# Performance work log

Hardware: AMD Instinct MI355X
Metric: run time of the kernel (lower is better)

Reference implementation:

```python
import jax, jax.numpy as jnp
import numpy as np

N = 4096
HID = 256
H = 4
D = HID // H  # 64
EDGE_DIM = 16
DEG = 32
E = N * DEG
EPS = 1e-5


def _layer_norm(x, g, b):
    m = jnp.mean(x, axis=-1, keepdims=True)
    v = jnp.mean((x - m) ** 2, axis=-1, keepdims=True)
    return (x - m) * jax.lax.rsqrt(v + EPS) * g + b


def setup_inputs() -> dict:
    key = jax.random.key(0)
    ks = jax.random.split(key, 16)
    s = 1.0 / np.sqrt(HID)
    x = jax.random.normal(ks[0], (N, HID), dtype=jnp.float32)
    # ring graph: every node is a src with DEG distinct neighbors -> no empty
    # softmax rows, no duplicate (src, dst) pairs
    src = jnp.repeat(jnp.arange(N, dtype=jnp.int64), DEG)
    dst = (src + jnp.tile(jnp.arange(1, DEG + 1, dtype=jnp.int64), N)) % N
    edge_index = jnp.stack([src, dst], axis=0)
    edge_attr = jax.random.normal(ks[1], (E, EDGE_DIM), dtype=jnp.float32)
    inp = {
        "x": x,
        "edge_index": edge_index,
        "edge_attr": edge_attr,
        "Wq": jax.random.uniform(ks[2], (HID, HID), jnp.float32, -s, s),
        "bq": jnp.zeros((HID,), jnp.float32),
        "Wk": jax.random.uniform(ks[3], (HID, HID), jnp.float32, -s, s),
        "bk": jnp.zeros((HID,), jnp.float32),
        "Wv": jax.random.uniform(ks[4], (HID, HID), jnp.float32, -s, s),
        "bv": jnp.zeros((HID,), jnp.float32),
        "Wo": jax.random.uniform(ks[5], (HID, HID), jnp.float32, -s, s),
        "bo": jnp.zeros((HID,), jnp.float32),
        "We": jax.random.uniform(ks[6], (EDGE_DIM, H), jnp.float32, -1.0 / np.sqrt(EDGE_DIM), 1.0 / np.sqrt(EDGE_DIM)),
        "be": jnp.zeros((H,), jnp.float32),
        "g1": jnp.ones((HID,), jnp.float32),
        "b1": jnp.zeros((HID,), jnp.float32),
        "g2": jnp.ones((HID,), jnp.float32),
        "b2": jnp.zeros((HID,), jnp.float32),
        "Wf1": jax.random.uniform(ks[7], (HID, 4 * HID), jnp.float32, -s, s),
        "bf1": jnp.zeros((4 * HID,), jnp.float32),
        "Wf2": jax.random.uniform(ks[8], (4 * HID, HID), jnp.float32, -1.0 / np.sqrt(4 * HID), 1.0 / np.sqrt(4 * HID)),
        "bf2": jnp.zeros((HID,), jnp.float32),
    }
    return inp


def reference(x, edge_index, edge_attr, Wq, bq, Wk, bk, Wv, bv, Wo, bo,
              We, be, g1, b1, g2, b2, Wf1, bf1, Wf2, bf2):
    src, dst = edge_index[0], edge_index[1]
    q = (x @ Wq + bq).reshape(N, H, D)
    k = (x @ Wk + bk).reshape(N, H, D)
    v = (x @ Wv + bv).reshape(N, H, D)
    edge_bias = edge_attr @ We + be                       # [E, H]
    dot = jnp.sum(q[src] * k[dst], axis=-1) / np.sqrt(D)  # [E, H]
    total_bias = dot + edge_bias                          # [E, H]
    # dense (H, N, N) logits, -inf everywhere except the E edges (as in the
    # original module)
    logits = jnp.full((H, N, N), -jnp.inf, dtype=x.dtype)
    logits = logits.at[:, src, dst].set(total_bias.T)
    attn = jax.nn.softmax(logits, axis=-1)                # [H, N, N]
    out = jnp.einsum('hnm,mhd->nhd', attn, v).reshape(N, HID)
    out = out @ Wo + bo
    x = _layer_norm(x + out, g1, b1)
    ffn = jax.nn.relu(x @ Wf1 + bf1) @ Wf2 + bf2
    x = _layer_norm(x + ffn, g2, b2)
    return x
```

## Files before the change

kernel.cpp:

```cpp
#include <hip/hip_runtime.h>
#include <cstddef>

#define N_NODES 4096
#define HIDDEN  256
#define NHEAD   4
#define DHEAD   64
#define EDGE_DIM 16
#define DEG     32
#define NEDGE   (N_NODES * DEG)
#define LN_EPS  1e-5f
#define QKV_STRIDE 768
#define KV_WIN  47

typedef short  s16x8 __attribute__((ext_vector_type(8)));
typedef float  f32x4 __attribute__((ext_vector_type(4)));
typedef unsigned short u16x8 __attribute__((ext_vector_type(8)));
typedef unsigned short u16x4 __attribute__((ext_vector_type(4)));

__device__ __forceinline__ unsigned short f2b(float f) {
    union { float f; unsigned u; } c{f};
    unsigned u = c.u;
    return (unsigned short)((u + 0x7fffu + ((u >> 16) & 1u)) >> 16);
}
__device__ __forceinline__ float b2f(unsigned short s) {
    union { unsigned u; float f; } c;
    c.u = ((unsigned)s) << 16;
    return c.f;
}
__device__ __forceinline__ int xcd_swz(int bid, int total) {
    const int q = total >> 3;
    return (bid & 7) * q + (bid >> 3);
}

__device__ __forceinline__ void pack_tile(const float* __restrict__ src,
                                          unsigned short* __restrict__ dst,
                                          int K, int Nn, int tt, int rowoff,
                                          float (*tile)[65], int tid) {
    const int tk = K / 64;
    const int k0 = (tt % tk) * 64, n0 = (tt / tk) * 64;

    const int kk = tid >> 2, nq = (tid & 3) * 16;
#pragma unroll
    for (int i = 0; i < 16; i += 4) {
        float4 vv = *(const float4*)&src[(size_t)(k0 + kk) * Nn + n0 + nq + i];
        tile[kk][nq + i + 0] = vv.x;
        tile[kk][nq + i + 1] = vv.y;
        tile[kk][nq + i + 2] = vv.z;
        tile[kk][nq + i + 3] = vv.w;
    }
    __syncthreads();
    const int nn = tid >> 2, kq = (tid & 3) * 16;
    unsigned short tmp[16];
#pragma unroll
    for (int i = 0; i < 16; ++i) tmp[i] = f2b(tile[kq + i][nn]);
    unsigned short* drow = dst + (size_t)(rowoff + n0 + nn) * K + k0 + kq;
    *(u16x8*)(drow + 0) = *(u16x8*)&tmp[0];
    *(u16x8*)(drow + 8) = *(u16x8*)&tmp[8];
}

__global__ __launch_bounds__(256) void pack_kernel(
    const float* __restrict__ Wq, const float* __restrict__ Wk,
    const float* __restrict__ Wv,
    const float* __restrict__ bq, const float* __restrict__ bk,
    const float* __restrict__ bv,
    unsigned short* __restrict__ Wqkv_t, float* __restrict__ bias768) {
    const int b = blockIdx.x;
    const int tid = threadIdx.x;
    __shared__ float tile[64][65];

    if (b < 48) {
        int m = b / 16, tt = b % 16;
        const float* src = (m == 0) ? Wq : ((m == 1) ? Wk : Wv);
        pack_tile(src, Wqkv_t, 256, 256, tt, m * 256, tile, tid);
    } else {
        bias768[tid]       = bq[tid];
        bias768[256 + tid] = bk[tid];
        bias768[512 + tid] = bv[tid];
    }
}

__global__ __launch_bounds__(256) void gemm_qkv(const float* __restrict__ X,
                                                const unsigned short* __restrict__ Bt,
                                                const float* __restrict__ bias,
                                                unsigned short* __restrict__ Cout,
                                                const float* __restrict__ Wo,
                                                const float* __restrict__ Wf1,
                                                const float* __restrict__ Wf2,
                                                unsigned short* __restrict__ Wo_t,
                                                unsigned short* __restrict__ Wf1_t,
                                                unsigned short* __restrict__ Wf2_t) {
    __shared__ __align__(16) char smem[64 * 65 * 4];
    const int bid = blockIdx.x;
    const int tid = threadIdx.x;

    if (bid >= 768) {
        float (*tile)[65] = (float(*)[65])smem;
        const int b2 = bid - 768;
        if (b2 < 16)       pack_tile(Wo,  Wo_t,  256,  256,  b2,      0, tile, tid);
        else if (b2 < 80)  pack_tile(Wf1, Wf1_t, 256,  1024, b2 - 16, 0, tile, tid);
        else               pack_tile(Wf2, Wf2_t, 1024, 256,  b2 - 80, 0, tile, tid);
        return;
    }

    unsigned short* sA = (unsigned short*)smem;
    unsigned short* sB = sA + 64 * 64;
    const int wave = tid >> 6, lane = tid & 63;
    const int b2 = xcd_swz(bid, 768);
    const int row0 = (b2 / 12) * 64, col0 = (b2 % 12) * 64;
    const int wr = wave >> 1, wc = wave & 1;

    f32x4 acc[2][2] = {};

    const int lo0 = tid * 16, lo1 = lo0 + 4096;
    const int r0 = lo0 >> 7, c0 = lo0 & 127;
    const int r1 = lo1 >> 7, c1 = lo1 & 127;
    const int so0 = (lo0 & ~127) | (c0 ^ ((r0 & 7) << 4));
    const int so1 = (lo1 & ~127) | (c1 ^ ((r1 & 7) << 4));

    const int ar  = tid >> 2;
    const int akb = (tid & 3) * 16;
    const int acb = akb * 2;
    const int axr = (ar & 7) << 4;
    const int aso0 = (ar * 128) | ((acb +  0) ^ axr);
    const int aso1 = (ar * 128) | ((acb + 16) ^ axr);

    float4 f0, f1, f2v, f3;
    s16x8 b0r, b1r;

#define QKV_LOAD(KT)                                                          \
    {                                                                         \
        const float* Ap = X + (size_t)(row0 + ar) * 256 + (KT) * 64 + akb;    \
        f0  = *(const float4*)(Ap + 0);                                       \
        f1  = *(const float4*)(Ap + 4);                                       \
        f2v = *(const float4*)(Ap + 8);                                       \
        f3  = *(const float4*)(Ap + 12);                                      \
        const char* Bb = (const char*)Bt + ((size_t)col0 * 256 + (KT) * 64) * 2; \
        b0r = *(const s16x8*)(Bb + (size_t)r0 * 512 + c0);                    \
        b1r = *(const s16x8*)(Bb + (size_t)r1 * 512 + c1);                    \
    }

    QKV_LOAD(0);
#pragma unroll
    for (int kt = 0; kt < 4; ++kt) {
        if (kt) __syncthreads();
        u16x8 pa0 = {f2b(f0.x), f2b(f0.y), f2b(f0.z), f2b(f0.w),
                     f2b(f1.x), f2b(f1.y), f2b(f1.z), f2b(f1.w)};
        u16x8 pa1 = {f2b(f2v.x), f2b(f2v.y), f2b(f2v.z), f2b(f2v.w),
                     f2b(f3.x), f2b(f3.y), f2b(f3.z), f2b(f3.w)};
        *(u16x8*)((char*)sA + aso0) = pa0;
        *(u16x8*)((char*)sA + aso1) = pa1;
        *(s16x8*)((char*)sB + so0) = b0r;
        *(s16x8*)((char*)sB + so1) = b1r;
        __syncthreads();
        if (kt < 3) QKV_LOAD(kt + 1);

        const char* sAc = (const char*)sA;
        const char* sBc = (const char*)sB;
#pragma unroll
        for (int kk = 0; kk < 64; kk += 32) {
            const int koffb = (kk + ((lane >> 4) << 3)) * 2;
            s16x8 a[2], bfr[2];
#pragma unroll
            for (int m = 0; m < 2; ++m) {
                const int r = wr * 32 + m * 16 + (lane & 15);
                int off = r * 128 + koffb;
                off ^= (r & 7) << 4;
                a[m] = *(const s16x8*)(sAc + off);
            }
#pragma unroll
            for (int n = 0; n < 2; ++n) {
                const int c = wc * 32 + n * 16 + (lane & 15);
                int off = c * 128 + koffb;
                off ^= (c & 7) << 4;
                bfr[n] = *(const s16x8*)(sBc + off);
            }
#pragma unroll
            for (int m = 0; m < 2; ++m)
#pragma unroll
                for (int n = 0; n < 2; ++n)
                    acc[m][n] = __builtin_amdgcn_mfma_f32_16x16x32_bf16(
                        a[m], bfr[n], acc[m][n], 0, 0, 0);
        }
    }
#undef QKV_LOAD

    const int crow = row0 + wr * 32 + ((lane >> 4) << 2);
    const int ccol = col0 + wc * 32 + (lane & 15);
#pragma unroll
    for (int n = 0; n < 2; ++n) {
        const int c = ccol + n * 16;
        const float bv = bias[c];
#pragma unroll
        for (int m = 0; m < 2; ++m)
#pragma unroll
            for (int j = 0; j < 4; ++j)
                Cout[(size_t)(crow + m * 16 + j) * QKV_STRIDE + c] =
                    f2b(acc[m][n][j] + bv);
    }
}

template <int K, bool RELU, bool OUTB>
__global__ __launch_bounds__(256) void gemm_mfma(const unsigned short* __restrict__ A,
                                                 const unsigned short* __restrict__ Bt,
                                                 const float* __restrict__ bias,
                                                 void* __restrict__ Cout,
                                                 int Nn, int nct, int total) {
    constexpr int NT = K / 64;
    __shared__ unsigned short sA[64 * 64];
    __shared__ unsigned short sB[64 * 64];
    const int tid = threadIdx.x;
    const int wave = tid >> 6, lane = tid & 63;
    const int b2 = xcd_swz(blockIdx.x, total);
    const int row0 = (b2 / nct) * 64, col0 = (b2 % nct) * 64;
    const int wr = wave >> 1, wc = wave & 1;

    f32x4 acc[2][2] = {};

    const int lo0 = tid * 16;
    const int lo1 = lo0 + 4096;
    const int r0 = lo0 >> 7, c0 = lo0 & 127;
    const int r1 = lo1 >> 7, c1 = lo1 & 127;
    const int so0 = (lo0 & ~127) | (c0 ^ ((r0 & 7) << 4));
    const int so1 = (lo1 & ~127) | (c1 ^ ((r1 & 7) << 4));

    s16x8 a0r, a1r, b0r, b1r;

#define GM_LOAD(KT)                                                           \
    {                                                                         \
        const char* Ab = (const char*)A + ((size_t)row0 * K + (KT) * 64) * 2; \
        const char* Bb = (const char*)Bt + ((size_t)col0 * K + (KT) * 64) * 2;\
        a0r = *(const s16x8*)(Ab + (size_t)r0 * (K * 2) + c0);                \
        a1r = *(const s16x8*)(Ab + (size_t)r1 * (K * 2) + c1);                \
        b0r = *(const s16x8*)(Bb + (size_t)r0 * (K * 2) + c0);                \
        b1r = *(const s16x8*)(Bb + (size_t)r1 * (K * 2) + c1);                \
    }

    GM_LOAD(0);
#pragma unroll
    for (int kt = 0; kt < NT; ++kt) {
        if (kt) __syncthreads();
        *(s16x8*)((char*)sA + so0) = a0r;
        *(s16x8*)((char*)sA + so1) = a1r;
        *(s16x8*)((char*)sB + so0) = b0r;
        *(s16x8*)((char*)sB + so1) = b1r;
        __syncthreads();
        if (kt + 1 < NT) GM_LOAD(kt + 1);

        const char* sAc = (const char*)sA;
        const char* sBc = (const char*)sB;
#pragma unroll
        for (int kk = 0; kk < 64; kk += 32) {
            const int koffb = (kk + ((lane >> 4) << 3)) * 2;
            s16x8 a[2], bfr[2];
#pragma unroll
            for (int m = 0; m < 2; ++m) {
                const int r = wr * 32 + m * 16 + (lane & 15);
                int off = r * 128 + koffb;
                off ^= (r & 7) << 4;
                a[m] = *(const s16x8*)(sAc + off);
            }
#pragma unroll
            for (int n = 0; n < 2; ++n) {
                const int c = wc * 32 + n * 16 + (lane & 15);
                int off = c * 128 + koffb;
                off ^= (c & 7) << 4;
                bfr[n] = *(const s16x8*)(sBc + off);
            }
#pragma unroll
            for (int m = 0; m < 2; ++m)
#pragma unroll
                for (int n = 0; n < 2; ++n)
                    acc[m][n] = __builtin_amdgcn_mfma_f32_16x16x32_bf16(
                        a[m], bfr[n], acc[m][n], 0, 0, 0);
        }
    }
#undef GM_LOAD

    const int crow = row0 + wr * 32 + ((lane >> 4) << 2);
    const int ccol = col0 + wc * 32 + (lane & 15);
#pragma unroll
    for (int n = 0; n < 2; ++n) {
        const int c = ccol + n * 16;
        const float bv = bias[c];
#pragma unroll
        for (int m = 0; m < 2; ++m) {
#pragma unroll
            for (int j = 0; j < 4; ++j) {
                const int r = crow + m * 16 + j;
                float v = acc[m][n][j] + bv;
                if (RELU) v = fmaxf(v, 0.f);
                if (OUTB)
                    ((unsigned short*)Cout)[(size_t)r * Nn + c] = f2b(v);
                else
                    ((float*)Cout)[(size_t)r * Nn + c] = v;
            }
        }
    }
}

__global__ __launch_bounds__(256) void gemm_partial(const unsigned short* __restrict__ A,
                                                    const unsigned short* __restrict__ Bt,
                                                    float* __restrict__ part) {
    constexpr int KF = 1024;
    __shared__ unsigned short sA[64 * 64];
    __shared__ unsigned short sB[64 * 64];
    const int tid = threadIdx.x;
    const int wave = tid >> 6, lane = tid & 63;
    const int b2 = xcd_swz(blockIdx.x, 512);
    const int z = b2 >> 8;
    const int rem = b2 & 255;
    const int row0 = (rem >> 2) * 64, col0 = (rem & 3) * 64;
    const int wr = wave >> 1, wc = wave & 1;

    f32x4 acc[2][2] = {};

    const int lo0 = tid * 16;
    const int lo1 = lo0 + 4096;
    const int r0 = lo0 >> 7, c0 = lo0 & 127;
    const int r1 = lo1 >> 7, c1 = lo1 & 127;
    const int so0 = (lo0 & ~127) | (c0 ^ ((r0 & 7) << 4));
    const int so1 = (lo1 & ~127) | (c1 ^ ((r1 & 7) << 4));

    const char* Abase = (const char*)A + ((size_t)row0 * KF + z * 512) * 2;
    const char* Bbase = (const char*)Bt + ((size_t)col0 * KF + z * 512) * 2;

    s16x8 a0r, a1r, b0r, b1r;

#define GP_LOAD(KT)                                                           \
    {                                                                         \
        a0r = *(const s16x8*)(Abase + (KT) * 128 + (size_t)r0 * (KF * 2) + c0); \
        a1r = *(const s16x8*)(Abase + (KT) * 128 + (size_t)r1 * (KF * 2) + c1); \
        b0r = *(const s16x8*)(Bbase + (KT) * 128 + (size_t)r0 * (KF * 2) + c0); \
        b1r = *(const s16x8*)(Bbase + (KT) * 128 + (size_t)r1 * (KF * 2) + c1); \
    }

    GP_LOAD(0);
#pragma unroll
    for (int kt = 0; kt < 8; ++kt) {
        if (kt) __syncthreads();
        *(s16x8*)((char*)sA + so0) = a0r;
        *(s16x8*)((char*)sA + so1) = a1r;
        *(s16x8*)((char*)sB + so0) = b0r;
        *(s16x8*)((char*)sB + so1) = b1r;
        __syncthreads();
        if (kt + 1 < 8) GP_LOAD(kt + 1);

        const char* sAc = (const char*)sA;
        const char* sBc = (const char*)sB;
#pragma unroll
        for (int kk = 0; kk < 64; kk += 32) {
            const int koffb = (kk + ((lane >> 4) << 3)) * 2;
            s16x8 a[2], bfr[2];
#pragma unroll
            for (int m = 0; m < 2; ++m) {
                const int r = wr * 32 + m * 16 + (lane & 15);
                int off = r * 128 + koffb;
                off ^= (r & 7) << 4;
                a[m] = *(const s16x8*)(sAc + off);
            }
#pragma unroll
            for (int n = 0; n < 2; ++n) {
                const int c = wc * 32 + n * 16 + (lane & 15);
                int off = c * 128 + koffb;
                off ^= (c & 7) << 4;
                bfr[n] = *(const s16x8*)(sBc + off);
            }
#pragma unroll
            for (int m = 0; m < 2; ++m)
#pragma unroll
                for (int n = 0; n < 2; ++n)
                    acc[m][n] = __builtin_amdgcn_mfma_f32_16x16x32_bf16(
                        a[m], bfr[n], acc[m][n], 0, 0, 0);
        }
    }
#undef GP_LOAD

    const int crow = row0 + wr * 32 + ((lane >> 4) << 2);
    const int ccol = col0 + wc * 32 + (lane & 15);
    float* pz = part + (size_t)z * N_NODES * HIDDEN;
#pragma unroll
    for (int n = 0; n < 2; ++n) {
        const int c = ccol + n * 16;
#pragma unroll
        for (int m = 0; m < 2; ++m)
#pragma unroll
            for (int j = 0; j < 4; ++j)
                pz[(size_t)(crow + m * 16 + j) * HIDDEN + c] = acc[m][n][j];
    }
}

__global__ __launch_bounds__(256) void ln2_reduce(const float* __restrict__ part,
                                                  const float* __restrict__ y,
                                                  const float* __restrict__ bf2,
                                                  const float* __restrict__ g2,
                                                  const float* __restrict__ b2,
                                                  float* __restrict__ out) {
    const int tid = threadIdx.x;
    const int row = blockIdx.x * 16 + (tid >> 4);
    const int cb = (tid & 15) * 16;
    const size_t rb = (size_t)row * HIDDEN;
    constexpr size_t ZS = (size_t)N_NODES * HIDDEN;

    float vals[16];
#pragma unroll
    for (int q = 0; q < 4; ++q) {
        const int c = cb + q * 4;
        float4 vy = *(const float4*)&y[rb + c];
        float4 vb = *(const float4*)&bf2[c];
        float4 s0 = *(const float4*)&part[0 * ZS + rb + c];
        float4 s1 = *(const float4*)&part[1 * ZS + rb + c];
        vals[q * 4 + 0] = vy.x + vb.x + s0.x + s1.x;
        vals[q * 4 + 1] = vy.y + vb.y + s0.y + s1.y;
        vals[q * 4 + 2] = vy.z + vb.z + s0.z + s1.z;
        vals[q * 4 + 3] = vy.w + vb.w + s0.w + s1.w;
    }
    float sm = 0.f, sq = 0.f;
#pragma unroll
    for (int i = 0; i < 16; ++i) { sm += vals[i]; sq = fmaf(vals[i], vals[i], sq); }
#pragma unroll
    for (int off = 8; off >= 1; off >>= 1) {
        sm += __shfl_xor(sm, off);
        sq += __shfl_xor(sq, off);
    }
    const float mean = sm * (1.f / HIDDEN);
    const float var  = sq * (1.f / HIDDEN) - mean * mean;
    const float inv  = rsqrtf(var + LN_EPS);
#pragma unroll
    for (int q = 0; q < 4; ++q) {
        const int c = cb + q * 4;
        float4 vg = *(const float4*)&g2[c];
        float4 vbb = *(const float4*)&b2[c];
        float4 o;
        o.x = (vals[q * 4 + 0] - mean) * inv * vg.x + vbb.x;
        o.y = (vals[q * 4 + 1] - mean) * inv * vg.y + vbb.y;
        o.z = (vals[q * 4 + 2] - mean) * inv * vg.z + vbb.z;
        o.w = (vals[q * 4 + 3] - mean) * inv * vg.w + vbb.w;
        *(float4*)&out[rb + c] = o;
    }
}

__global__ __launch_bounds__(512) void attn_oproj_ln(
    const unsigned short* __restrict__ qkv,
    const int* __restrict__ edge_dst,
    const float* __restrict__ edge_attr,
    const float* __restrict__ We, const float* __restrict__ be,
    const unsigned short* __restrict__ Wo_t,
    const float* __restrict__ bo,
    const float* __restrict__ x,
    const float* __restrict__ g, const float* __restrict__ b,
    float* __restrict__ y, unsigned short* __restrict__ yb) {
    __shared__ float sQ[16][260];
    __shared__ float sP[16][NHEAD][DEG];
    __shared__ int   sDst[16][DEG];
    __shared__ float sWe[EDGE_DIM * NHEAD];
    __shared__ unsigned short sKV[2][KV_WIN * 256];
    __shared__ unsigned short sA[16 * 256];
    __shared__ unsigned short sB[2][256 * 64];
    __shared__ float rs[16][8], rq[16][8];

    const int tid = threadIdx.x;
    const int wave = tid >> 6, lane = tid & 63;
    const int n0 = blockIdx.x * 16;

    {
        const int r = tid >> 5, e = (tid & 31) * 8;
        u16x8 v = *(const u16x8*)(qkv + (size_t)(n0 + r) * QKV_STRIDE + e);
#pragma unroll
        for (int i = 0; i < 8; ++i) sQ[r][e + i] = b2f(v[i]);
    }
    for (int t = tid; t < 2 * KV_WIN * 32; t += 512) {
        const int half = (t >= KV_WIN * 32) ? 1 : 0;
        const int tt = t - half * (KV_WIN * 32);
        const int rr = tt >> 5, c16 = tt & 31;
        const int gsrc = (n0 + 1 + rr) & (N_NODES - 1);
        u16x8 v = *(const u16x8*)(qkv + (size_t)gsrc * QKV_STRIDE +
                                  (half ? 512 : 256) + c16 * 8);
        const int so = rr * 512 + ((c16 ^ (rr & 7)) * 16);
        *(u16x8*)((char*)sKV[half] + so) = v;
    }
    if (tid < EDGE_DIM * NHEAD) sWe[tid] = We[tid];
    __syncthreads();

    {
        const int node = tid >> 5, j = tid & 31;
        const int dstj = edge_dst[(n0 + node) * DEG + j];
        sDst[node][j] = dstj;
        const int idx = (dstj - n0 - 1) & (N_NODES - 1);
        const char* krow = (const char*)sKV[0] + idx * 512;
        const int swz = (idx & 7);
        float lg[4];
#pragma unroll
        for (int h = 0; h < 4; ++h) {
            float dot = 0.f;
            const float* qh = &sQ[node][h * 64];
#pragma unroll
            for (int q8 = 0; q8 < 8; ++q8) {
                const int c16 = h * 8 + q8;
                u16x8 kv = *(const u16x8*)(krow + ((c16 ^ swz) * 16));
#pragma unroll
                for (int d = 0; d < 8; ++d)
                    dot = fmaf(qh[q8 * 8 + d], b2f(kv[d]), dot);
            }
            lg[h] = dot * 0.125f + be[h];
        }
        const float* ea_ = edge_attr + (size_t)((n0 + node) * DEG + j) * EDGE_DIM;
#pragma unroll
        for (int c = 0; c < EDGE_DIM; ++c) {
            const float eav = ea_[c];
#pragma unroll
            for (int h = 0; h < 4; ++h)
                lg[h] = fmaf(eav, sWe[c * NHEAD + h], lg[h]);
        }
#pragma unroll
        for (int h = 0; h < 4; ++h) {
            float mx = lg[h];
#pragma unroll
            for (int off = 16; off >= 1; off >>= 1)
                mx = fmaxf(mx, __shfl_xor(mx, off));
            float p = __expf(lg[h] - mx);
            float sum = p;
#pragma unroll
            for (int off = 16; off >= 1; off >>= 1)
                sum += __shfl_xor(sum, off);
            sP[node][h][j] = p / sum;
        }
    }
    __syncthreads();

    {
        const int node = tid >> 5, oct = tid & 31;
        const int h = oct >> 3;
        const int chunk = oct;
        float acc8[8] = {};
#pragma unroll 8
        for (int j = 0; j < DEG; ++j) {
            const float p = sP[node][h][j];
            const int idx = (sDst[node][j] - n0 - 1) & (N_NODES - 1);
            u16x8 vv = *(const u16x8*)((const char*)sKV[1] + idx * 512 +
                                       ((chunk ^ (idx & 7)) * 16));
#pragma unroll
            for (int i = 0; i < 8; ++i) acc8[i] = fmaf(p, b2f(vv[i]), acc8[i]);
        }
        u16x8 pk;
#pragma unroll
        for (int i = 0; i < 8; ++i) pk[i] = f2b(acc8[i]);
        const int so = node * 512 + ((oct * 16) ^ ((node & 7) << 4));
        *(u16x8*)((char*)sA + so) = pk;
    }

    s16x8 breg[4];
#define WO_LOAD(KT)                                                           \
    {                                                                         \
        _Pragma("unroll")                                                     \
        for (int p = 0; p < 4; ++p) {                                         \
            const int lo = tid * 16 + p * 8192;                               \
            const int r = lo >> 7, c = lo & 127;                              \
            breg[p] = *(const s16x8*)((const char*)Wo_t + (size_t)r * 512 +   \
                                      (KT) * 128 + c);                        \
        }                                                                     \
    }
#define WO_STORE(BUF)                                                         \
    {                                                                         \
        _Pragma("unroll")                                                     \
        for (int p = 0; p < 4; ++p) {                                         \
            const int lo = tid * 16 + p * 8192;                               \
            const int r = lo >> 7, c = lo & 127;                              \
            const int so = (lo & ~127) | (c ^ ((r & 7) << 4));                \
            *(s16x8*)((char*)sB[BUF] + so) = breg[p];                         \
        }                                                                     \
    }

    WO_LOAD(0);
    WO_STORE(0);
    __syncthreads();

    f32x4 acc[2] = {};
#pragma unroll
    for (int kt = 0; kt < 4; ++kt) {
        if (kt + 1 < 4) WO_LOAD(kt + 1);

        const char* sBc = (const char*)sB[kt & 1];
#pragma unroll
        for (int kk = 0; kk < 64; kk += 32) {
            const int lk = ((lane >> 4) << 3);
            s16x8 a;
            {
                const int r = lane & 15;
                const int koffb = (kt * 64 + kk + lk) * 2;
                a = *(const s16x8*)((const char*)sA + r * 512 +
                                    (koffb ^ ((r & 7) << 4)));
            }
            s16x8 bfr[2];
            const int boffb = (kk + lk) * 2;
#pragma unroll
            for (int n = 0; n < 2; ++n) {
                const int c = wave * 32 + n * 16 + (lane & 15);
                bfr[n] = *(const s16x8*)(sBc + c * 128 + (boffb ^ ((c & 7) << 4)));
            }
#pragma unroll
            for (int n = 0; n < 2; ++n)
                acc[n] = __builtin_amdgcn_mfma_f32_16x16x32_bf16(a, bfr[n], acc[n], 0, 0, 0);
        }

        if (kt + 1 < 4) {
            WO_STORE((kt + 1) & 1);
            __syncthreads();
        }
    }
#undef WO_LOAD
#undef WO_STORE

    const int rbase = ((lane >> 4) << 2);
    const int cbase = wave * 32 + (lane & 15);

    float sm[4] = {}, sq_[4] = {};
#pragma unroll
    for (int n = 0; n < 2; ++n) {
        const int c = cbase + n * 16;
        const float bv = bo[c];
#pragma unroll
        for (int j = 0; j < 4; ++j) {
            const int r = rbase + j;
            float v = acc[n][j] + bv + x[(size_t)(n0 + r) * HIDDEN + c];
            acc[n][j] = v;
            sm[j] += v;
            sq_[j] = fmaf(v, v, sq_[j]);
        }
    }
#pragma unroll
    for (int off = 8; off >= 1; off >>= 1) {
#pragma unroll
        for (int j = 0; j < 4; ++j) {
            sm[j] += __shfl_xor(sm[j], off);
            sq_[j] += __shfl_xor(sq_[j], off);
        }
    }
    if ((lane & 15) == 0) {
#pragma unroll
        for (int j = 0; j < 4; ++j) {
            rs[rbase + j][wave] = sm[j];
            rq[rbase + j][wave] = sq_[j];
        }
    }
    __syncthreads();

#pragma unroll
    for (int j = 0; j < 4; ++j) {
        const int r = rbase + j;
        float tot = 0.f, totq = 0.f;
#pragma unroll
        for (int w = 0; w < 8; ++w) { tot += rs[r][w]; totq += rq[r][w]; }
        const float mean = tot * (1.f / HIDDEN);
        const float var  = totq * (1.f / HIDDEN) - mean * mean;
        const float inv  = rsqrtf(var + LN_EPS);
#pragma unroll
        for (int n = 0; n < 2; ++n) {
            const int c = cbase + n * 16;
            const float res = (acc[n][j] - mean) * inv * g[c] + b[c];
            y[(size_t)(n0 + r) * HIDDEN + c] = res;
            yb[(size_t)(n0 + r) * HIDDEN + c] = f2b(res);
        }
    }
}

extern "C" void kernel_launch(void* const* d_in, const int* in_sizes, int n_in,
                              void* d_out, int out_size, void* d_ws, size_t ws_size,
                              hipStream_t stream) {
    const float* x   = (const float*)d_in[0];
    const int*   ei  = (const int*)d_in[1];
    const float* ea  = (const float*)d_in[2];
    const float* Wq  = (const float*)d_in[3];
    const float* bq  = (const float*)d_in[4];
    const float* Wk  = (const float*)d_in[5];
    const float* bk  = (const float*)d_in[6];
    const float* Wv  = (const float*)d_in[7];
    const float* bv  = (const float*)d_in[8];
    const float* Wo  = (const float*)d_in[9];
    const float* bo  = (const float*)d_in[10];
    const float* We  = (const float*)d_in[11];
    const float* be  = (const float*)d_in[12];
    const float* g1  = (const float*)d_in[13];
    const float* b1  = (const float*)d_in[14];
    const float* g2  = (const float*)d_in[15];
    const float* b2  = (const float*)d_in[16];
    const float* Wf1 = (const float*)d_in[17];
    const float* bf1 = (const float*)d_in[18];
    const float* Wf2 = (const float*)d_in[19];
    const float* bf2 = (const float*)d_in[20];

    char* W = (char*)d_ws;
    unsigned short* Wqkv_t  = (unsigned short*)(W + (2u << 20));
    unsigned short* Wo_t    = (unsigned short*)(W + (2u << 20) + 384 * 1024);
    unsigned short* Wf1_t   = (unsigned short*)(W + (2u << 20) + 512 * 1024);
    unsigned short* Wf2_t   = (unsigned short*)(W + (2u << 20) + 1024 * 1024);
    float*          bias768 = (float*)(W + (2u << 20) + 1536 * 1024);
    unsigned short* qkvb    = (unsigned short*)(W + (4u << 20));
    unsigned short* h1b     = (unsigned short*)(W + (4u << 20));
    float*          y       = (float*)(W + (12u << 20));
    unsigned short* yb      = (unsigned short*)(W + (16u << 20));
    float*          part    = (float*)(W + (20u << 20));

    const dim3 blk(256);

    pack_kernel<<<49, blk, 0, stream>>>(Wq, Wk, Wv, bq, bk, bv, Wqkv_t, bias768);

    gemm_qkv<<<912, blk, 0, stream>>>(x, Wqkv_t, bias768, qkvb,
                                      Wo, Wf1, Wf2, Wo_t, Wf1_t, Wf2_t);

    attn_oproj_ln<<<N_NODES / 16, dim3(512), 0, stream>>>(
        qkvb, ei + NEDGE, ea, We, be, Wo_t, bo, x, g1, b1, y, yb);

    gemm_mfma<256, true, true><<<1024, blk, 0, stream>>>(
        yb, Wf1_t, bf1, h1b, 4 * HIDDEN, 16, 1024);

    gemm_partial<<<512, blk, 0, stream>>>(h1b, Wf2_t, part);

    ln2_reduce<<<N_NODES / 16, blk, 0, stream>>>(part, y, bf2, g2, b2, (float*)d_out);
}
```

Baseline: 55.54 us.

## Move weight packing to pack kernel, widen FFN1 tiles, finer LN2 rows

All weight transposes (Wo, Wf1, Wf2) now happen in the pack kernel instead of extra blocks inside the QKV GEMM, so the QKV GEMM gets a smaller LDS footprint and only launches GEMM blocks. The FFN1 GEMM becomes a dedicated kernel with 64x128 tiles (2x4 MFMA tiles per wave), halving block count and increasing B-operand reuse per A load. The LN2 reduce kernel uses 32 threads per row with 8 values each, doubling the block count for more parallelism. The cost is more register pressure in FFN1 and the pack kernel running serially ahead of the QKV GEMM with more blocks.

```diff
diff --git a/kernel.cpp b/kernel.cpp
--- a/kernel.cpp
+++ b/kernel.cpp
@@ -60,10 +60,13 @@
 
 __global__ __launch_bounds__(256) void pack_kernel(
     const float* __restrict__ Wq, const float* __restrict__ Wk,
-    const float* __restrict__ Wv,
+    const float* __restrict__ Wv, const float* __restrict__ Wo,
+    const float* __restrict__ Wf1, const float* __restrict__ Wf2,
     const float* __restrict__ bq, const float* __restrict__ bk,
     const float* __restrict__ bv,
-    unsigned short* __restrict__ Wqkv_t, float* __restrict__ bias768) {
+    unsigned short* __restrict__ Wqkv_t, unsigned short* __restrict__ Wo_t,
+    unsigned short* __restrict__ Wf1_t, unsigned short* __restrict__ Wf2_t,
+    float* __restrict__ bias768) {
     const int b = blockIdx.x;
     const int tid = threadIdx.x;
     __shared__ float tile[64][65];
@@ -72,6 +75,12 @@
         int m = b / 16, tt = b % 16;
         const float* src = (m == 0) ? Wq : ((m == 1) ? Wk : Wv);
         pack_tile(src, Wqkv_t, 256, 256, tt, m * 256, tile, tid);
+    } else if (b < 64) {
+        pack_tile(Wo, Wo_t, 256, 256, b - 48, 0, tile, tid);
+    } else if (b < 128) {
+        pack_tile(Wf1, Wf1_t, 256, 1024, b - 64, 0, tile, tid);
+    } else if (b < 192) {
+        pack_tile(Wf2, Wf2_t, 1024, 256, b - 128, 0, tile, tid);
     } else {
         bias768[tid]       = bq[tid];
         bias768[256 + tid] = bk[tid];
@@ -82,30 +91,12 @@
 __global__ __launch_bounds__(256) void gemm_qkv(const float* __restrict__ X,
                                                 const unsigned short* __restrict__ Bt,
                                                 const float* __restrict__ bias,
-                                                unsigned short* __restrict__ Cout,
-                                                const float* __restrict__ Wo,
-                                                const float* __restrict__ Wf1,
-                                                const float* __restrict__ Wf2,
-                                                unsigned short* __restrict__ Wo_t,
-                                                unsigned short* __restrict__ Wf1_t,
-                                                unsigned short* __restrict__ Wf2_t) {
-    __shared__ __align__(16) char smem[64 * 65 * 4];
-    const int bid = blockIdx.x;
+                                                unsigned short* __restrict__ Cout) {
+    __shared__ unsigned short sA[64 * 64];
+    __shared__ unsigned short sB[64 * 64];
     const int tid = threadIdx.x;
-
-    if (bid >= 768) {
-        float (*tile)[65] = (float(*)[65])smem;
-        const int b2 = bid - 768;
-        if (b2 < 16)       pack_tile(Wo,  Wo_t,  256,  256,  b2,      0, tile, tid);
-        else if (b2 < 80)  pack_tile(Wf1, Wf1_t, 256,  1024, b2 - 16, 0, tile, tid);
-        else               pack_tile(Wf2, Wf2_t, 1024, 256,  b2 - 80, 0, tile, tid);
-        return;
-    }
-
-    unsigned short* sA = (unsigned short*)smem;
-    unsigned short* sB = sA + 64 * 64;
     const int wave = tid >> 6, lane = tid & 63;
-    const int b2 = xcd_swz(bid, 768);
+    const int b2 = xcd_swz(blockIdx.x, 768);
     const int row0 = (b2 / 12) * 64, col0 = (b2 % 12) * 64;
     const int wr = wave >> 1, wc = wave & 1;
 
@@ -199,59 +190,65 @@
     }
 }
 
-template <int K, bool RELU, bool OUTB>
-__global__ __launch_bounds__(256) void gemm_mfma(const unsigned short* __restrict__ A,
+__global__ __launch_bounds__(256) void gemm_ffn1(const unsigned short* __restrict__ A,
                                                  const unsigned short* __restrict__ Bt,
                                                  const float* __restrict__ bias,
-                                                 void* __restrict__ Cout,
-                                                 int Nn, int nct, int total) {
-    constexpr int NT = K / 64;
+                                                 unsigned short* __restrict__ Cout) {
+    constexpr int K = 256;
     __shared__ unsigned short sA[64 * 64];
-    __shared__ unsigned short sB[64 * 64];
+    __shared__ unsigned short sB[128 * 64];
     const int tid = threadIdx.x;
     const int wave = tid >> 6, lane = tid & 63;
-    const int b2 = xcd_swz(blockIdx.x, total);
-    const int row0 = (b2 / nct) * 64, col0 = (b2 % nct) * 64;
+    const int b2 = xcd_swz(blockIdx.x, 512);
+    const int row0 = (b2 >> 3) * 64, col0 = (b2 & 7) * 128;
     const int wr = wave >> 1, wc = wave & 1;
 
-    f32x4 acc[2][2] = {};
-
-    const int lo0 = tid * 16;
-    const int lo1 = lo0 + 4096;
+    f32x4 acc[2][4] = {};
+
+    const int lo0 = tid * 16, lo1 = lo0 + 4096;
     const int r0 = lo0 >> 7, c0 = lo0 & 127;
     const int r1 = lo1 >> 7, c1 = lo1 & 127;
     const int so0 = (lo0 & ~127) | (c0 ^ ((r0 & 7) << 4));
     const int so1 = (lo1 & ~127) | (c1 ^ ((r1 & 7) << 4));
 
-    s16x8 a0r, a1r, b0r, b1r;
-
-#define GM_LOAD(KT)                                                           \
+    s16x8 a0r, a1r, breg[4];
+
+#define F1_LOAD(KT)                                                           \
     {                                                                         \
         const char* Ab = (const char*)A + ((size_t)row0 * K + (KT) * 64) * 2; \
-        const char* Bb = (const char*)Bt + ((size_t)col0 * K + (KT) * 64) * 2;\
         a0r = *(const s16x8*)(Ab + (size_t)r0 * (K * 2) + c0);                \
         a1r = *(const s16x8*)(Ab + (size_t)r1 * (K * 2) + c1);                \
-        b0r = *(const s16x8*)(Bb + (size_t)r0 * (K * 2) + c0);                \
-        b1r = *(const s16x8*)(Bb + (size_t)r1 * (K * 2) + c1);                \
-    }
-
-    GM_LOAD(0);
-#pragma unroll
-    for (int kt = 0; kt < NT; ++kt) {
+        const char* Bb = (const char*)Bt + ((size_t)col0 * K + (KT) * 64) * 2;\
+        _Pragma("unroll")                                                     \
+        for (int p = 0; p < 4; ++p) {                                         \
+            const int lo = tid * 16 + p * 4096;                               \
+            const int r = lo >> 7, c = lo & 127;                              \
+            breg[p] = *(const s16x8*)(Bb + (size_t)r * (K * 2) + c);          \
+        }                                                                     \
+    }
+
+    F1_LOAD(0);
+#pragma unroll
+    for (int kt = 0; kt < 4; ++kt) {
         if (kt) __syncthreads();
         *(s16x8*)((char*)sA + so0) = a0r;
         *(s16x8*)((char*)sA + so1) = a1r;
-        *(s16x8*)((char*)sB + so0) = b0r;
-        *(s16x8*)((char*)sB + so1) = b1r;
+#pragma unroll
+        for (int p = 0; p < 4; ++p) {
+            const int lo = tid * 16 + p * 4096;
+            const int r = lo >> 7, c = lo & 127;
+            const int so = (lo & ~127) | (c ^ ((r & 7) << 4));
+            *(s16x8*)((char*)sB + so) = breg[p];
+        }
         __syncthreads();
-        if (kt + 1 < NT) GM_LOAD(kt + 1);
+        if (kt + 1 < 4) F1_LOAD(kt + 1);
 
         const char* sAc = (const char*)sA;
         const char* sBc = (const char*)sB;
 #pragma unroll
         for (int kk = 0; kk < 64; kk += 32) {
             const int koffb = (kk + ((lane >> 4) << 3)) * 2;
-            s16x8 a[2], bfr[2];
+            s16x8 a[2], bfr[4];
 #pragma unroll
             for (int m = 0; m < 2; ++m) {
                 const int r = wr * 32 + m * 16 + (lane & 15);
@@ -260,8 +257,8 @@
                 a[m] = *(const s16x8*)(sAc + off);
             }
 #pragma unroll
-            for (int n = 0; n < 2; ++n) {
-                const int c = wc * 32 + n * 16 + (lane & 15);
+            for (int n = 0; n < 4; ++n) {
+                const int c = wc * 64 + n * 16 + (lane & 15);
                 int off = c * 128 + koffb;
                 off ^= (c & 7) << 4;
                 bfr[n] = *(const s16x8*)(sBc + off);
@@ -269,32 +266,26 @@
 #pragma unroll
             for (int m = 0; m < 2; ++m)
 #pragma unroll
-                for (int n = 0; n < 2; ++n)
+                for (int n = 0; n < 4; ++n)
                     acc[m][n] = __builtin_amdgcn_mfma_f32_16x16x32_bf16(
                         a[m], bfr[n], acc[m][n], 0, 0, 0);
         }
     }
-#undef GM_LOAD
+#undef F1_LOAD
 
     const int crow = row0 + wr * 32 + ((lane >> 4) << 2);
-    const int ccol = col0 + wc * 32 + (lane & 15);
-#pragma unroll
-    for (int n = 0; n < 2; ++n) {
+    const int ccol = col0 + wc * 64 + (lane & 15);
+#pragma unroll
+    for (int n = 0; n < 4; ++n) {
         const int c = ccol + n * 16;
         const float bv = bias[c];
 #pragma unroll
-        for (int m = 0; m < 2; ++m) {
+        for (int m = 0; m < 2; ++m)
 #pragma unroll
             for (int j = 0; j < 4; ++j) {
                 const int r = crow + m * 16 + j;
-                float v = acc[m][n][j] + bv;
-                if (RELU) v = fmaxf(v, 0.f);
-                if (OUTB)
-                    ((unsigned short*)Cout)[(size_t)r * Nn + c] = f2b(v);
-                else
-                    ((float*)Cout)[(size_t)r * Nn + c] = v;
-            }
-        }
+                Cout[(size_t)r * 1024 + c] = f2b(fmaxf(acc[m][n][j] + bv, 0.f));
+            }
     }
 }
 
@@ -396,14 +387,14 @@
                                                   const float* __restrict__ b2,
                                                   float* __restrict__ out) {
     const int tid = threadIdx.x;
-    const int row = blockIdx.x * 16 + (tid >> 4);
-    const int cb = (tid & 15) * 16;
+    const int row = blockIdx.x * 8 + (tid >> 5);
+    const int cb = (tid & 31) * 8;
     const size_t rb = (size_t)row * HIDDEN;
     constexpr size_t ZS = (size_t)N_NODES * HIDDEN;
 
-    float vals[16];
-#pragma unroll
-    for (int q = 0; q < 4; ++q) {
+    float vals[8];
+#pragma unroll
+    for (int q = 0; q < 2; ++q) {
         const int c = cb + q * 4;
         float4 vy = *(const float4*)&y[rb + c];
         float4 vb = *(const float4*)&bf2[c];
@@ -416,9 +407,9 @@
     }
     float sm = 0.f, sq = 0.f;
 #pragma unroll
-    for (int i = 0; i < 16; ++i) { sm += vals[i]; sq = fmaf(vals[i], vals[i], sq); }
-#pragma unroll
-    for (int off = 8; off >= 1; off >>= 1) {
+    for (int i = 0; i < 8; ++i) { sm += vals[i]; sq = fmaf(vals[i], vals[i], sq); }
+#pragma unroll
+    for (int off = 16; off >= 1; off >>= 1) {
         sm += __shfl_xor(sm, off);
         sq += __shfl_xor(sq, off);
     }
@@ -426,7 +417,7 @@
     const float var  = sq * (1.f / HIDDEN) - mean * mean;
     const float inv  = rsqrtf(var + LN_EPS);
 #pragma unroll
-    for (int q = 0; q < 4; ++q) {
+    for (int q = 0; q < 2; ++q) {
         const int c = cb + q * 4;
         float4 vg = *(const float4*)&g2[c];
         float4 vbb = *(const float4*)&b2[c];
@@ -702,18 +693,17 @@
 
     const dim3 blk(256);
 
-    pack_kernel<<<49, blk, 0, stream>>>(Wq, Wk, Wv, bq, bk, bv, Wqkv_t, bias768);
-
-    gemm_qkv<<<912, blk, 0, stream>>>(x, Wqkv_t, bias768, qkvb,
-                                      Wo, Wf1, Wf2, Wo_t, Wf1_t, Wf2_t);
+    pack_kernel<<<193, blk, 0, stream>>>(Wq, Wk, Wv, Wo, Wf1, Wf2, bq, bk, bv,
+                                         Wqkv_t, Wo_t, Wf1_t, Wf2_t, bias768);
+
+    gemm_qkv<<<768, blk, 0, stream>>>(x, Wqkv_t, bias768, qkvb);
 
     attn_oproj_ln<<<N_NODES / 16, dim3(512), 0, stream>>>(
         qkvb, ei + NEDGE, ea, We, be, Wo_t, bo, x, g1, b1, y, yb);
 
-    gemm_mfma<256, true, true><<<1024, blk, 0, stream>>>(
-        yb, Wf1_t, bf1, h1b, 4 * HIDDEN, 16, 1024);
+    gemm_ffn1<<<512, blk, 0, stream>>>(yb, Wf1_t, bf1, h1b);
 
     gemm_partial<<<512, blk, 0, stream>>>(h1b, Wf2_t, part);
 
-    ln2_reduce<<<N_NODES / 16, blk, 0, stream>>>(part, y, bf2, g2, b2, (float*)d_out);
-}
+    ln2_reduce<<<N_NODES / 8, blk, 0, stream>>>(part, y, bf2, g2, b2, (float*)d_out);
+}
```

Result: faster. 53.76 us (-3.2%).
